# Kernel tuning notes

Measured on AMD Instinct MI355X. Metric: run time of the kernel, lower is better.

Reference implementation:

```python
import jax, jax.numpy as jnp
import numpy as np

DECAY = 0.99
LR = 0.01

def setup_inputs() -> dict:
    key = jax.random.key(0)
    ks = jax.random.split(key, 6)
    B, S, D, M = 4, 4096, 1024, 128
    sD = 1.0 / np.sqrt(D)
    sM = 1.0 / np.sqrt(M)
    return {
        "x": jax.random.normal(ks[0], (B, S, D), dtype=jnp.float32),
        "Wk": jax.random.uniform(ks[1], (M, D), jnp.float32, -sD, sD),
        "bk": jnp.zeros((M,), jnp.float32),
        "Wv": jax.random.uniform(ks[2], (M, D), jnp.float32, -sD, sD),
        "bv": jnp.zeros((M,), jnp.float32),
        "Wq": jax.random.uniform(ks[3], (M, D), jnp.float32, -sD, sD),
        "bq": jnp.zeros((M,), jnp.float32),
        "Wo": jax.random.uniform(ks[4], (D, M), jnp.float32, -sM, sM),
        "bo": jnp.zeros((D,), jnp.float32),
    }

def reference(x, Wk, bk, Wv, bv, Wq, bq, Wo, bo):
    B, S, D = x.shape
    M = Wk.shape[0]
    # Precompute all projections in one batched GEMM each: [B,S,M]
    k = jnp.einsum('bsd,md->bsm', x, Wk) + bk
    v = jnp.einsum('bsd,md->bsm', x, Wv) + bv
    q = jnp.einsum('bsd,md->bsm', x, Wq) + bq

    def step(state, kvq):
        k_t, v_t, q_t = kvq  # each [B, M]
        # readout uses the PRE-update state, matching the torch loop order
        out_t = jnp.einsum('bij,bj->bi', state, q_t)          # [B, M]
        state = DECAY * state + LR * jnp.einsum('bi,bj->bij', v_t, k_t)
        return state, out_t

    state0 = jnp.zeros((B, M, M), x.dtype)
    # scan over time: move seq axis to front -> [S, B, M]
    xs = (jnp.swapaxes(k, 0, 1), jnp.swapaxes(v, 0, 1), jnp.swapaxes(q, 0, 1))
    state, outs = jax.lax.scan(step, state0, xs)
    outs = jnp.swapaxes(outs, 0, 1)                            # [B, S, M]
    y = jnp.einsum('bsm,dm->bsd', outs, Wo) + bo               # [B, S, D]
    return (y, state)
```

## Files before the change

### kernel.cpp

```cpp
#include <hip/hip_runtime.h>
#include <math.h>

namespace {
constexpr int kB = 4;
constexpr int kS = 4096;
constexpr int kD = 1024;
constexpr int kM = 128;
constexpr int kC = 64;
constexpr int kNC = kS / kC;
constexpr int kRS = kB * kS;
constexpr float kLR = 0.01f;
constexpr float kLog2d = -0.0144995696f;
}

typedef __bf16 bf16x8 __attribute__((ext_vector_type(8)));
typedef float  f32x4  __attribute__((ext_vector_type(4)));
typedef unsigned short u16;
typedef unsigned int   u32;

__device__ __forceinline__ u16 f2bf(float f) {
  u32 x = __float_as_uint(f);
  u32 r = (x + 0x7fffu + ((x >> 16) & 1u)) >> 16;
  return (u16)r;
}

__device__ __forceinline__ float bf2f(u16 h) {
  return __uint_as_float(((u32)h) << 16);
}

__device__ __forceinline__ void gl_lds16(const void* g, void* l) {
  __builtin_amdgcn_global_load_lds(
      (const __attribute__((address_space(1))) void*)g,
      (__attribute__((address_space(3))) void*)l, 16, 0, 0);
}

__device__ __forceinline__ f32x4 mf(bf16x8 a, bf16x8 b, f32x4 c) {
  return __builtin_amdgcn_mfma_f32_16x16x32_bf16(a, b, c, 0, 0, 0);
}

__global__ __launch_bounds__(256)
void cast_w_kernel(const float* __restrict__ Wk, const float* __restrict__ Wv,
                   const float* __restrict__ Wq, const float* __restrict__ Wo,
                   u16* __restrict__ Wkvq, u16* __restrict__ Woh)
{
  int i = (blockIdx.x * 256 + threadIdx.x) * 4;
  const float* src;
  u16* dst;
  if (i < 393216) {
    src = (i < 131072) ? Wk + i : (i < 262144) ? Wv + (i - 131072) : Wq + (i - 262144);
    dst = Wkvq + i;
  } else {
    src = Wo + (i - 393216);
    dst = Woh + (i - 393216);
  }
  float4 v = *(const float4*)src;
  ushort4 o;
  o.x = f2bf(v.x); o.y = f2bf(v.y); o.z = f2bf(v.z); o.w = f2bf(v.w);
  *(ushort4*)dst = o;
}

__global__ __launch_bounds__(256)
void fused_proj_intra(const float* __restrict__ x, const u16* __restrict__ Wkvq,
                      const float* __restrict__ bk, const float* __restrict__ bv,
                      const float* __restrict__ bq,
                      u16* __restrict__ Qg, u16* __restrict__ O1g,
                      float* __restrict__ SU)
{
  __shared__ __align__(16) u16 L[32768];
  const int c = blockIdx.x, b = blockIdx.y;
  const int R0 = b * kS + c * kC;
  const int tid = threadIdx.x, w = tid >> 6, lane = tid & 63;
  const int fr = lane & 15, qd = lane >> 4;

  f32x4 acc[4][6] = {};
  const int xrow = tid >> 2, xcol = (tid & 3) * 8;
  const float* xp = x + (size_t)(R0 + xrow) * kD + xcol;
  u16* asDst = &L[xrow * 32 + xcol];
  const u16* wp = Wkvq + (size_t)(96 * w + (lane >> 2)) * kD + (lane & 3) * 8;
  u16* bsDst = &L[2048 + (96 * w) * 32];

  float4 xa = *(const float4*)xp;
  float4 xb = *(const float4*)(xp + 4);
  for (int k0 = 0; k0 < kD; k0 += 32) {
    __syncthreads();
#pragma unroll
    for (int i = 0; i < 6; ++i)
      gl_lds16(wp + k0 + (size_t)(i * 16) * kD, bsDst + i * 512);
    u16 xh8[8];
    xh8[0] = f2bf(xa.x); xh8[1] = f2bf(xa.y); xh8[2] = f2bf(xa.z); xh8[3] = f2bf(xa.w);
    xh8[4] = f2bf(xb.x); xh8[5] = f2bf(xb.y); xh8[6] = f2bf(xb.z); xh8[7] = f2bf(xb.w);
    *(uint4*)asDst = *(uint4*)xh8;
    __syncthreads();
    if (k0 + 32 < kD) {
      xa = *(const float4*)(xp + k0 + 32);
      xb = *(const float4*)(xp + k0 + 36);
    }
    bf16x8 av[4], bvv[6];
#pragma unroll
    for (int mi = 0; mi < 4; ++mi)
      av[mi] = *(const bf16x8*)&L[(mi * 16 + fr) * 32 + qd * 8];
#pragma unroll
    for (int nj = 0; nj < 6; ++nj)
      bvv[nj] = *(const bf16x8*)&L[2048 + (96 * w + nj * 16 + fr) * 32 + qd * 8];
#pragma unroll
    for (int mi = 0; mi < 4; ++mi)
#pragma unroll
      for (int nj = 0; nj < 6; ++nj)
        acc[mi][nj] = mf(av[mi], bvv[nj], acc[mi][nj]);
  }
  __syncthreads();

  float dp63[16];
#pragma unroll
  for (int mi = 0; mi < 4; ++mi)
#pragma unroll
    for (int r = 0; r < 4; ++r)
      dp63[mi * 4 + r] = kLR * exp2f((float)(63 - (mi * 16 + qd * 4 + r)) * kLog2d);

#pragma unroll
  for (int nj = 0; nj < 6; ++nj) {
    const int n = 96 * w + nj * 16 + fr;
    const int slab = n >> 7, j = n & 127;
    const float* bp = (slab == 0) ? bk : (slab == 1) ? bv : bq;
    const float bias = bp[j];
#pragma unroll
    for (int mi = 0; mi < 4; ++mi)
#pragma unroll
      for (int r = 0; r < 4; ++r) {
        const int t = mi * 16 + qd * 4 + r;
        const float val = acc[mi][nj][r] + bias;
        const u16 h = f2bf(val);
        if (slab == 0) {
          L[8192 + (j >> 5) * 2048 + t * 32 + (j & 31)] = h;
          L[24576 + (t >> 5) * 4096 + j * 32 + (t & 31)] = f2bf(val * dp63[mi * 4 + r]);
        } else if (slab == 1) {
          L[16384 + (t >> 5) * 4096 + j * 32 + (t & 31)] = h;
        } else {
          L[(j >> 5) * 2048 + t * 32 + (j & 31)] = h;
          Qg[(size_t)(R0 + t) * kM + j] = h;
        }
      }
  }
  __syncthreads();

  const int mP = (w >> 1) * 32, nP = (w & 1) * 32;
  f32x4 p[2][2] = {};
#pragma unroll
  for (int kp = 0; kp < 4; ++kp) {
    bf16x8 a2[2], b2[2];
#pragma unroll
    for (int mi = 0; mi < 2; ++mi)
      a2[mi] = *(const bf16x8*)&L[kp * 2048 + (mP + mi * 16 + fr) * 32 + qd * 8];
#pragma unroll
    for (int ni = 0; ni < 2; ++ni)
      b2[ni] = *(const bf16x8*)&L[8192 + kp * 2048 + (nP + ni * 16 + fr) * 32 + qd * 8];
#pragma unroll
    for (int mi = 0; mi < 2; ++mi)
#pragma unroll
      for (int ni = 0; ni < 2; ++ni)
        p[mi][ni] = mf(a2[mi], b2[ni], p[mi][ni]);
  }
  __syncthreads();

#pragma unroll
  for (int mi = 0; mi < 2; ++mi)
#pragma unroll
    for (int r = 0; r < 4; ++r) {
      const int t = mP + mi * 16 + qd * 4 + r;
#pragma unroll
      for (int ni = 0; ni < 2; ++ni) {
        const int u = nP + ni * 16 + fr;
        float av2 = 0.f;
        if (u < t) av2 = kLR * exp2f((float)(t - 1 - u) * kLog2d) * p[mi][ni][r];
        L[8192 + (u >> 5) * 2048 + t * 32 + (u & 31)] = f2bf(av2);
      }
    }
  __syncthreads();

  const int mO = (w >> 1) * 32, nO = (w & 1) * 64;
  const int mU = (w >> 1) * 64, nU = (w & 1) * 64;
  f32x4 o1[2][4] = {}, uu[4][4] = {};
#pragma unroll
  for (int kp = 0; kp < 2; ++kp) {
    bf16x8 af[2], vb[4], va[4], ub[4];
#pragma unroll
    for (int mi = 0; mi < 2; ++mi)
      af[mi] = *(const bf16x8*)&L[8192 + kp * 2048 + (mO + mi * 16 + fr) * 32 + qd * 8];
#pragma unroll
    for (int ni = 0; ni < 4; ++ni)
      vb[ni] = *(const bf16x8*)&L[16384 + kp * 4096 + (nO + ni * 16 + fr) * 32 + qd * 8];
#pragma unroll
    for (int mi = 0; mi < 4; ++mi)
      va[mi] = *(const bf16x8*)&L[16384 + kp * 4096 + (mU + mi * 16 + fr) * 32 + qd * 8];
#pragma unroll
    for (int ni = 0; ni < 4; ++ni)
      ub[ni] = *(const bf16x8*)&L[24576 + kp * 4096 + (nU + ni * 16 + fr) * 32 + qd * 8];
#pragma unroll
    for (int mi = 0; mi < 2; ++mi)
#pragma unroll
      for (int ni = 0; ni < 4; ++ni)
        o1[mi][ni] = mf(af[mi], vb[ni], o1[mi][ni]);
#pragma unroll
    for (int mi = 0; mi < 4; ++mi)
#pragma unroll
      for (int ni = 0; ni < 4; ++ni)
        uu[mi][ni] = mf(va[mi], ub[ni], uu[mi][ni]);
  }

#pragma unroll
  for (int mi = 0; mi < 2; ++mi)
#pragma unroll
    for (int ni = 0; ni < 4; ++ni)
#pragma unroll
      for (int r = 0; r < 4; ++r) {
        const int t = mO + mi * 16 + qd * 4 + r, i = nO + ni * 16 + fr;
        O1g[(size_t)(R0 + t) * kM + i] = f2bf(o1[mi][ni][r]);
      }
  float* SUc = SU + (size_t)(b * kNC + c) * (kM * kM);
#pragma unroll
  for (int mi = 0; mi < 4; ++mi)
#pragma unroll
    for (int ni = 0; ni < 4; ++ni)
#pragma unroll
      for (int r = 0; r < 4; ++r) {
        const int i = mU + mi * 16 + qd * 4 + r, j = nU + ni * 16 + fr;
        SUc[i * kM + j] = uu[mi][ni][r];
      }
}

__global__ __launch_bounds__(256)
void scan_kernel(const float* __restrict__ SU, u16* __restrict__ Sb16,
                 float* __restrict__ state_out)
{
  const int e = blockIdx.x * 256 + threadIdx.x;
  const int b = e >> 14, ij = e & 16383;
  const float* base = SU + (size_t)b * kNC * 16384 + ij;
  u16* sb = Sb16 + (size_t)b * kNC * 16384 + ij;
  const float dC = exp2f((float)kC * kLog2d);
  float prev = 0.f;
#pragma unroll 8
  for (int c2 = 0; c2 < kNC; ++c2) {
    const float u = base[(size_t)c2 * 16384];
    sb[(size_t)c2 * 16384] = f2bf(prev);
    prev = fmaf(dC, prev, u);
  }
  state_out[e] = prev;
}

__global__ __launch_bounds__(256)
void fused_combine_out(const u16* __restrict__ Qg, const u16* __restrict__ Sb16,
                       const u16* __restrict__ O1g, const u16* __restrict__ Woh,
                       const float* __restrict__ bo, float* __restrict__ y)
{
  __shared__ __align__(16) u16 L[24576];
  const int c = blockIdx.x, b = blockIdx.y;
  const int R0 = b * kS + c * kC;
  const int tid = threadIdx.x, w = tid >> 6, lane = tid & 63;
  const int fr = lane & 15, qd = lane >> 4;
  const size_t cbS = (size_t)(b * kNC + c) * 16384;

  {
    const u16* gq = Qg + (size_t)(R0 + (lane >> 2)) * kM + w * 32 + (lane & 3) * 8;
    u16* lq = &L[w * 2048];
#pragma unroll
    for (int g = 0; g < 4; ++g)
      gl_lds16(gq + (size_t)(g * 16) * kM, lq + g * 512);
    const u16* gs = Sb16 + cbS + (size_t)(lane >> 2) * kM + w * 32 + (lane & 3) * 8;
    u16* ls = &L[8192 + w * 4096];
#pragma unroll
    for (int g = 0; g < 8; ++g)
      gl_lds16(gs + (size_t)(g * 16) * kM, ls + g * 512);
  }

  const int mO = (w >> 1) * 32, nO = (w & 1) * 64;
  u16 o1h[2][4][4];
#pragma unroll
  for (int mi = 0; mi < 2; ++mi)
#pragma unroll
    for (int ni = 0; ni < 4; ++ni)
#pragma unroll
      for (int r = 0; r < 4; ++r)
        o1h[mi][ni][r] =
            O1g[(size_t)(R0 + mO + mi * 16 + qd * 4 + r) * kM + nO + ni * 16 + fr];
  __syncthreads();

  f32x4 o2[2][4] = {};
#pragma unroll
  for (int kp = 0; kp < 4; ++kp) {
    bf16x8 aq[2], bs[4];
#pragma unroll
    for (int mi = 0; mi < 2; ++mi)
      aq[mi] = *(const bf16x8*)&L[kp * 2048 + (mO + mi * 16 + fr) * 32 + qd * 8];
#pragma unroll
    for (int ni = 0; ni < 4; ++ni)
      bs[ni] = *(const bf16x8*)&L[8192 + kp * 4096 + (nO + ni * 16 + fr) * 32 + qd * 8];
#pragma unroll
    for (int mi = 0; mi < 2; ++mi)
#pragma unroll
      for (int ni = 0; ni < 4; ++ni)
        o2[mi][ni] = mf(aq[mi], bs[ni], o2[mi][ni]);
  }
  __syncthreads();

#pragma unroll
  for (int mi = 0; mi < 2; ++mi)
#pragma unroll
    for (int r = 0; r < 4; ++r) {
      const int t = mO + mi * 16 + qd * 4 + r;
      const float dt = exp2f((float)t * kLog2d);
#pragma unroll
      for (int ni = 0; ni < 4; ++ni) {
        const int i = nO + ni * 16 + fr;
        const float ov = fmaf(dt, o2[mi][ni][r], bf2f(o1h[mi][ni][r]));
        L[(i >> 5) * 2048 + t * 32 + (i & 31)] = f2bf(ov);
      }
    }
  __syncthreads();

#pragma unroll 1
  for (int h = 0; h < 2; ++h) {
    const int n0 = w * 256 + h * 128;
    f32x4 fy[4][8] = {};
#pragma unroll
    for (int kp = 0; kp < 4; ++kp) {
      bf16x8 ao[4], bw[8];
#pragma unroll
      for (int mi = 0; mi < 4; ++mi)
        ao[mi] = *(const bf16x8*)&L[kp * 2048 + (mi * 16 + fr) * 32 + qd * 8];
#pragma unroll
      for (int nj = 0; nj < 8; ++nj)
        bw[nj] = *(const bf16x8*)&Woh[(size_t)(n0 + nj * 16 + fr) * kM + kp * 32 + qd * 8];
#pragma unroll
      for (int mi = 0; mi < 4; ++mi)
#pragma unroll
        for (int nj = 0; nj < 8; ++nj)
          fy[mi][nj] = mf(ao[mi], bw[nj], fy[mi][nj]);
    }
#pragma unroll
    for (int nj = 0; nj < 8; ++nj) {
      const int d = n0 + nj * 16 + fr;
      const float bb = bo[d];
#pragma unroll
      for (int mi = 0; mi < 4; ++mi)
#pragma unroll
        for (int r = 0; r < 4; ++r)
          y[(size_t)(R0 + mi * 16 + qd * 4 + r) * kD + d] = fy[mi][nj][r] + bb;
    }
  }
}

extern "C" void kernel_launch(void* const* d_in, const int* in_sizes, int n_in,
                              void* d_out, int out_size, void* d_ws, size_t ws_size,
                              hipStream_t stream) {
  const float* x  = (const float*)d_in[0];
  const float* Wk = (const float*)d_in[1];
  const float* bk = (const float*)d_in[2];
  const float* Wv = (const float*)d_in[3];
  const float* bv = (const float*)d_in[4];
  const float* Wq = (const float*)d_in[5];
  const float* bq = (const float*)d_in[6];
  const float* Wo = (const float*)d_in[7];
  const float* bo = (const float*)d_in[8];

  char* wsp = (char*)d_ws;
  u16* Wkvq = (u16*)wsp;   wsp += (size_t)384 * 1024 * 2;
  u16* Woh  = (u16*)wsp;   wsp += (size_t)1024 * 128 * 2;
  u16* Qg   = (u16*)wsp;   wsp += (size_t)kRS * kM * 2;
  u16* O1g  = (u16*)wsp;   wsp += (size_t)kRS * kM * 2;
  float* SU = (float*)wsp; wsp += (size_t)kB * kNC * 16384 * 4;
  u16* Sb16 = (u16*)wsp;   wsp += (size_t)kB * kNC * 16384 * 2;

  float* y = (float*)d_out;
  float* state_out = y + (size_t)kRS * kD;

  dim3 blk(256);
  cast_w_kernel<<<dim3(512), blk, 0, stream>>>(Wk, Wv, Wq, Wo, Wkvq, Woh);
  fused_proj_intra<<<dim3(kNC, kB), blk, 0, stream>>>(x, Wkvq, bk, bv, bq, Qg, O1g, SU);
  scan_kernel<<<dim3(kB * 16384 / 256), blk, 0, stream>>>(SU, Sb16, state_out);
  fused_combine_out<<<dim3(kNC, kB), blk, 0, stream>>>(Qg, Sb16, O1g, Woh, bo, y);
}
```

Baseline: 189.6 us.

## Split fused projection and combine kernels into finer-grained kernels with fragment layouts

Splits the fused projection+intra-chunk kernel into a projection GEMM with a 256x3 grid that is double-buffered in LDS, plus a separate intra-chunk kernel. It also splits combine+output into a combine kernel and an out-projection GEMM on an 8x128 grid. Intermediates are stored in an MFMA-fragment-ordered layout so the consumer kernels can load them straight into LDS. The aim is more blocks per launch and better pipelining than the 256-block fused kernels. The cost is extra launches and more global round trips for Q, K, V and the intermediate outputs.

```diff
diff --git a/kernel.cpp b/kernel.cpp
--- a/kernel.cpp
+++ b/kernel.cpp
@@ -8,6 +8,7 @@
 constexpr int kM = 128;
 constexpr int kC = 64;
 constexpr int kNC = kS / kC;
+constexpr int kNCG = kB * kNC;
 constexpr int kRS = kB * kS;
 constexpr float kLR = 0.01f;
 constexpr float kLog2d = -0.0144995696f;
@@ -36,6 +37,22 @@
 
 __device__ __forceinline__ f32x4 mf(bf16x8 a, bf16x8 b, f32x4 c) {
   return __builtin_amdgcn_mfma_f32_16x16x32_bf16(a, b, c, 0, 0, 0);
+}
+
+__device__ __forceinline__ ushort4 pack4(float4 a) {
+  ushort4 o;
+  o.x = f2bf(a.x); o.y = f2bf(a.y); o.z = f2bf(a.z); o.w = f2bf(a.w);
+  return o;
+}
+
+__device__ __forceinline__ int fo64x128(int r, int c) {
+  return ((r >> 4) * 4 + (c >> 5)) * 1024 + ((c >> 3) & 3) * 256 + (r & 15) * 16 + (c & 7) * 2;
+}
+__device__ __forceinline__ int fo128x64(int r, int c) {
+  return ((r >> 4) * 2 + (c >> 5)) * 1024 + ((c >> 3) & 3) * 256 + (r & 15) * 16 + (c & 7) * 2;
+}
+__device__ __forceinline__ int fo64x64(int r, int c) {
+  return ((r >> 4) * 2 + (c >> 5)) * 1024 + ((c >> 3) & 3) * 256 + (r & 15) * 16 + (c & 7) * 2;
 }
 
 __global__ __launch_bounds__(256)
@@ -54,177 +71,221 @@
     dst = Woh + (i - 393216);
   }
   float4 v = *(const float4*)src;
-  ushort4 o;
-  o.x = f2bf(v.x); o.y = f2bf(v.y); o.z = f2bf(v.z); o.w = f2bf(v.w);
-  *(ushort4*)dst = o;
-}
-
-__global__ __launch_bounds__(256)
-void fused_proj_intra(const float* __restrict__ x, const u16* __restrict__ Wkvq,
-                      const float* __restrict__ bk, const float* __restrict__ bv,
-                      const float* __restrict__ bq,
-                      u16* __restrict__ Qg, u16* __restrict__ O1g,
-                      float* __restrict__ SU)
-{
-  __shared__ __align__(16) u16 L[32768];
-  const int c = blockIdx.x, b = blockIdx.y;
-  const int R0 = b * kS + c * kC;
+  *(ushort4*)dst = pack4(v);
+}
+
+__global__ __launch_bounds__(256, 3)
+void proj_gemm(const float* __restrict__ x, const u16* __restrict__ Wkvq,
+               const float* __restrict__ bk, const float* __restrict__ bv,
+               const float* __restrict__ bq,
+               u16* __restrict__ Qg, u16* __restrict__ Kg,
+               u16* __restrict__ VTg, u16* __restrict__ KwTg)
+{
+  __shared__ __align__(16) u16 L[24576];
+  const int cg = blockIdx.x, s = blockIdx.y;
+  const int R0 = cg * 64;
   const int tid = threadIdx.x, w = tid >> 6, lane = tid & 63;
   const int fr = lane & 15, qd = lane >> 4;
-
-  f32x4 acc[4][6] = {};
-  const int xrow = tid >> 2, xcol = (tid & 3) * 8;
-  const float* xp = x + (size_t)(R0 + xrow) * kD + xcol;
-  u16* asDst = &L[xrow * 32 + xcol];
-  const u16* wp = Wkvq + (size_t)(96 * w + (lane >> 2)) * kD + (lane & 3) * 8;
-  u16* bsDst = &L[2048 + (96 * w) * 32];
-
-  float4 xa = *(const float4*)xp;
-  float4 xb = *(const float4*)(xp + 4);
-  for (int k0 = 0; k0 < kD; k0 += 32) {
+  const int wr = w >> 1, wc = w & 1;
+
+  constexpr int A0 = 0, A1o = 8192, B0 = 16384, B1o = 32768;
+
+  const int xr = tid >> 2, s4 = tid & 3;
+  const float* xp = x + (size_t)(R0 + xr) * kD + s4 * 4;
+  int aoffq[4];
+#pragma unroll
+  for (int q = 0; q < 4; ++q)
+    aoffq[q] = ((xr >> 4) * 2 + (q >> 1)) * 1024 + (((s4 >> 1) + 2 * q) & 3) * 256
+             + (xr & 15) * 16 + (s4 & 1) * 8;
+
+  const u16* wbase = Wkvq + (size_t)(128 * s) * kD + qd * 8;
+
+  f32x4 acc[2][4] = {};
+  float4 xv[4];
+
+  {
+#pragma unroll
+    for (int g = 0; g < 4; ++g) {
+      const int pn = 4 * w + g, ng = pn >> 1, kh = pn & 1;
+      gl_lds16(wbase + (size_t)(ng * 16 + fr) * kD + kh * 32, &L[(B0 + pn * 1024) >> 1]);
+    }
+    float4 x0[4];
+#pragma unroll
+    for (int q = 0; q < 4; ++q) x0[q] = *(const float4*)(xp + q * 16);
+#pragma unroll
+    for (int q = 0; q < 4; ++q) *(ushort4*)&L[(A0 + aoffq[q]) >> 1] = pack4(x0[q]);
+#pragma unroll
+    for (int q = 0; q < 4; ++q) xv[q] = *(const float4*)(xp + 64 + q * 16);
+  }
+  __syncthreads();
+
+#pragma unroll 2
+  for (int i = 0; i < 16; ++i) {
+    const int Ac = (i & 1) ? A1o : A0, Bc = (i & 1) ? B1o : B0;
+    const int An = (i & 1) ? A0 : A1o, Bn = (i & 1) ? B0 : B1o;
+    if (i < 15) {
+      const int k1 = (i + 1) * 64;
+#pragma unroll
+      for (int g = 0; g < 4; ++g) {
+        const int pn = 4 * w + g, ng = pn >> 1, kh = pn & 1;
+        gl_lds16(wbase + (size_t)(ng * 16 + fr) * kD + k1 + kh * 32, &L[(Bn + pn * 1024) >> 1]);
+      }
+#pragma unroll
+      for (int q = 0; q < 4; ++q) *(ushort4*)&L[(An + aoffq[q]) >> 1] = pack4(xv[q]);
+      if (i < 14) {
+#pragma unroll
+        for (int q = 0; q < 4; ++q) xv[q] = *(const float4*)(xp + (i + 2) * 64 + q * 16);
+      }
+    }
+    bf16x8 af[2][2], bfr[2][4];
+#pragma unroll
+    for (int kh = 0; kh < 2; ++kh) {
+#pragma unroll
+      for (int mi = 0; mi < 2; ++mi)
+        af[kh][mi] = *(const bf16x8*)&L[(Ac + ((wr * 2 + mi) * 2 + kh) * 1024 + qd * 256 + fr * 16) >> 1];
+#pragma unroll
+      for (int ng = 0; ng < 4; ++ng)
+        bfr[kh][ng] = *(const bf16x8*)&L[(Bc + ((wc * 4 + ng) * 2 + kh) * 1024 + qd * 256 + fr * 16) >> 1];
+    }
+#pragma unroll
+    for (int kh = 0; kh < 2; ++kh)
+#pragma unroll
+      for (int mi = 0; mi < 2; ++mi)
+#pragma unroll
+        for (int ng = 0; ng < 4; ++ng)
+          acc[mi][ng] = mf(af[kh][mi], bfr[kh][ng], acc[mi][ng]);
     __syncthreads();
-#pragma unroll
-    for (int i = 0; i < 6; ++i)
-      gl_lds16(wp + k0 + (size_t)(i * 16) * kD, bsDst + i * 512);
-    u16 xh8[8];
-    xh8[0] = f2bf(xa.x); xh8[1] = f2bf(xa.y); xh8[2] = f2bf(xa.z); xh8[3] = f2bf(xa.w);
-    xh8[4] = f2bf(xb.x); xh8[5] = f2bf(xb.y); xh8[6] = f2bf(xb.z); xh8[7] = f2bf(xb.w);
-    *(uint4*)asDst = *(uint4*)xh8;
-    __syncthreads();
-    if (k0 + 32 < kD) {
-      xa = *(const float4*)(xp + k0 + 32);
-      xb = *(const float4*)(xp + k0 + 36);
-    }
-    bf16x8 av[4], bvv[6];
-#pragma unroll
-    for (int mi = 0; mi < 4; ++mi)
-      av[mi] = *(const bf16x8*)&L[(mi * 16 + fr) * 32 + qd * 8];
-#pragma unroll
-    for (int nj = 0; nj < 6; ++nj)
-      bvv[nj] = *(const bf16x8*)&L[2048 + (96 * w + nj * 16 + fr) * 32 + qd * 8];
-#pragma unroll
-    for (int mi = 0; mi < 4; ++mi)
-#pragma unroll
-      for (int nj = 0; nj < 6; ++nj)
-        acc[mi][nj] = mf(av[mi], bvv[nj], acc[mi][nj]);
-  }
-  __syncthreads();
-
-  float dp63[16];
-#pragma unroll
-  for (int mi = 0; mi < 4; ++mi)
-#pragma unroll
-    for (int r = 0; r < 4; ++r)
-      dp63[mi * 4 + r] = kLR * exp2f((float)(63 - (mi * 16 + qd * 4 + r)) * kLog2d);
-
-#pragma unroll
-  for (int nj = 0; nj < 6; ++nj) {
-    const int n = 96 * w + nj * 16 + fr;
-    const int slab = n >> 7, j = n & 127;
-    const float* bp = (slab == 0) ? bk : (slab == 1) ? bv : bq;
-    const float bias = bp[j];
-#pragma unroll
-    for (int mi = 0; mi < 4; ++mi)
+  }
+
+  const float* bp = (s == 0) ? bk : (s == 1) ? bv : bq;
+  float bias[4];
+#pragma unroll
+  for (int ng = 0; ng < 4; ++ng) bias[ng] = bp[wc * 64 + ng * 16 + fr];
+  const size_t cb = (size_t)cg * 8192;
+
+  if (s == 0) {
+    float dp[2][4];
+#pragma unroll
+    for (int mi = 0; mi < 2; ++mi)
+#pragma unroll
+      for (int r = 0; r < 4; ++r)
+        dp[mi][r] = kLR * exp2f((float)(63 - (wr * 32 + mi * 16 + qd * 4 + r)) * kLog2d);
+#pragma unroll
+    for (int mi = 0; mi < 2; ++mi)
+#pragma unroll
+      for (int ng = 0; ng < 4; ++ng)
+#pragma unroll
+        for (int r = 0; r < 4; ++r) {
+          const int t = wr * 32 + mi * 16 + qd * 4 + r, n = wc * 64 + ng * 16 + fr;
+          const float v = acc[mi][ng][r] + bias[ng];
+          Kg[cb + (fo64x128(t, n) >> 1)] = f2bf(v);
+          KwTg[cb + (fo128x64(n, t) >> 1)] = f2bf(v * dp[mi][r]);
+        }
+  } else if (s == 1) {
+#pragma unroll
+    for (int mi = 0; mi < 2; ++mi)
+#pragma unroll
+      for (int ng = 0; ng < 4; ++ng)
+#pragma unroll
+        for (int r = 0; r < 4; ++r) {
+          const int t = wr * 32 + mi * 16 + qd * 4 + r, n = wc * 64 + ng * 16 + fr;
+          VTg[cb + (fo128x64(n, t) >> 1)] = f2bf(acc[mi][ng][r] + bias[ng]);
+        }
+  } else {
+#pragma unroll
+    for (int mi = 0; mi < 2; ++mi)
+#pragma unroll
+      for (int ng = 0; ng < 4; ++ng)
+#pragma unroll
+        for (int r = 0; r < 4; ++r) {
+          const int t = wr * 32 + mi * 16 + qd * 4 + r, n = wc * 64 + ng * 16 + fr;
+          Qg[cb + (fo64x128(t, n) >> 1)] = f2bf(acc[mi][ng][r] + bias[ng]);
+        }
+  }
+}
+
+__global__ __launch_bounds__(256, 2)
+void intra_kernel(const u16* __restrict__ Qg, const u16* __restrict__ Kg,
+                  const u16* __restrict__ VTg, const u16* __restrict__ KwTg,
+                  u16* __restrict__ O1g, float* __restrict__ SU)
+{
+  __shared__ __align__(16) u16 L[32768];
+  const int cg = blockIdx.x;
+  const int tid = threadIdx.x, w = tid >> 6, lane = tid & 63;
+  const int fr = lane & 15, qd = lane >> 4;
+  const size_t cb = (size_t)cg * 8192;
+
+#pragma unroll
+  for (int g = 0; g < 4; ++g) {
+    const int pn = 4 * w + g;
+    gl_lds16(Qg + cb + pn * 512 + lane * 8, &L[(0 + pn * 1024) >> 1]);
+    gl_lds16(Kg + cb + pn * 512 + lane * 8, &L[(16384 + pn * 1024) >> 1]);
+    gl_lds16(VTg + cb + pn * 512 + lane * 8, &L[(32768 + pn * 1024) >> 1]);
+    gl_lds16(KwTg + cb + pn * 512 + lane * 8, &L[(49152 + pn * 1024) >> 1]);
+  }
+  __syncthreads();
+
+  f32x4 p[4] = {};
+#pragma unroll
+  for (int kc = 0; kc < 4; ++kc) {
+    bf16x8 aq = *(const bf16x8*)&L[(0 + (w * 4 + kc) * 1024 + qd * 256 + fr * 16) >> 1];
+#pragma unroll
+    for (int ug = 0; ug < 4; ++ug) {
+      bf16x8 bkf = *(const bf16x8*)&L[(16384 + (ug * 4 + kc) * 1024 + qd * 256 + fr * 16) >> 1];
+      p[ug] = mf(aq, bkf, p[ug]);
+    }
+  }
+  __syncthreads();
+
+#pragma unroll
+  for (int ug = 0; ug < 4; ++ug)
+#pragma unroll
+    for (int r = 0; r < 4; ++r) {
+      const int t = w * 16 + qd * 4 + r, u = ug * 16 + fr;
+      float av = 0.f;
+      if (u < t) av = kLR * exp2f((float)(t - 1 - u) * kLog2d) * p[ug][r];
+      L[(0 + fo64x64(t, u)) >> 1] = f2bf(av);
+    }
+  __syncthreads();
+
+  f32x4 o1[8] = {}, uu[2][8] = {};
+#pragma unroll
+  for (int h = 0; h < 2; ++h) {
+    bf16x8 aA = *(const bf16x8*)&L[(0 + (w * 2 + h) * 1024 + qd * 256 + fr * 16) >> 1];
+    bf16x8 aV[2];
+#pragma unroll
+    for (int mi = 0; mi < 2; ++mi)
+      aV[mi] = *(const bf16x8*)&L[(32768 + ((2 * w + mi) * 2 + h) * 1024 + qd * 256 + fr * 16) >> 1];
+#pragma unroll
+    for (int ig = 0; ig < 8; ++ig) {
+      bf16x8 bV = *(const bf16x8*)&L[(32768 + (ig * 2 + h) * 1024 + qd * 256 + fr * 16) >> 1];
+      o1[ig] = mf(aA, bV, o1[ig]);
+    }
+#pragma unroll
+    for (int jg = 0; jg < 8; ++jg) {
+      bf16x8 bK = *(const bf16x8*)&L[(49152 + (jg * 2 + h) * 1024 + qd * 256 + fr * 16) >> 1];
+#pragma unroll
+      for (int mi = 0; mi < 2; ++mi)
+        uu[mi][jg] = mf(aV[mi], bK, uu[mi][jg]);
+    }
+  }
+
+#pragma unroll
+  for (int ig = 0; ig < 8; ++ig)
+#pragma unroll
+    for (int r = 0; r < 4; ++r) {
+      const int t = w * 16 + qd * 4 + r, i2 = ig * 16 + fr;
+      O1g[cb + (fo64x128(t, i2) >> 1)] = f2bf(o1[ig][r]);
+    }
+  float* SUc = SU + (size_t)cg * 16384;
+#pragma unroll
+  for (int mi = 0; mi < 2; ++mi)
+#pragma unroll
+    for (int jg = 0; jg < 8; ++jg)
 #pragma unroll
       for (int r = 0; r < 4; ++r) {
-        const int t = mi * 16 + qd * 4 + r;
-        const float val = acc[mi][nj][r] + bias;
-        const u16 h = f2bf(val);
-        if (slab == 0) {
-          L[8192 + (j >> 5) * 2048 + t * 32 + (j & 31)] = h;
-          L[24576 + (t >> 5) * 4096 + j * 32 + (t & 31)] = f2bf(val * dp63[mi * 4 + r]);
-        } else if (slab == 1) {
-          L[16384 + (t >> 5) * 4096 + j * 32 + (t & 31)] = h;
-        } else {
-          L[(j >> 5) * 2048 + t * 32 + (j & 31)] = h;
-          Qg[(size_t)(R0 + t) * kM + j] = h;
-        }
-      }
-  }
-  __syncthreads();
-
-  const int mP = (w >> 1) * 32, nP = (w & 1) * 32;
-  f32x4 p[2][2] = {};
-#pragma unroll
-  for (int kp = 0; kp < 4; ++kp) {
-    bf16x8 a2[2], b2[2];
-#pragma unroll
-    for (int mi = 0; mi < 2; ++mi)
-      a2[mi] = *(const bf16x8*)&L[kp * 2048 + (mP + mi * 16 + fr) * 32 + qd * 8];
-#pragma unroll
-    for (int ni = 0; ni < 2; ++ni)
-      b2[ni] = *(const bf16x8*)&L[8192 + kp * 2048 + (nP + ni * 16 + fr) * 32 + qd * 8];
-#pragma unroll
-    for (int mi = 0; mi < 2; ++mi)
-#pragma unroll
-      for (int ni = 0; ni < 2; ++ni)
-        p[mi][ni] = mf(a2[mi], b2[ni], p[mi][ni]);
-  }
-  __syncthreads();
-
-#pragma unroll
-  for (int mi = 0; mi < 2; ++mi)
-#pragma unroll
-    for (int r = 0; r < 4; ++r) {
-      const int t = mP + mi * 16 + qd * 4 + r;
-#pragma unroll
-      for (int ni = 0; ni < 2; ++ni) {
-        const int u = nP + ni * 16 + fr;
-        float av2 = 0.f;
-        if (u < t) av2 = kLR * exp2f((float)(t - 1 - u) * kLog2d) * p[mi][ni][r];
-        L[8192 + (u >> 5) * 2048 + t * 32 + (u & 31)] = f2bf(av2);
-      }
-    }
-  __syncthreads();
-
-  const int mO = (w >> 1) * 32, nO = (w & 1) * 64;
-  const int mU = (w >> 1) * 64, nU = (w & 1) * 64;
-  f32x4 o1[2][4] = {}, uu[4][4] = {};
-#pragma unroll
-  for (int kp = 0; kp < 2; ++kp) {
-    bf16x8 af[2], vb[4], va[4], ub[4];
-#pragma unroll
-    for (int mi = 0; mi < 2; ++mi)
-      af[mi] = *(const bf16x8*)&L[8192 + kp * 2048 + (mO + mi * 16 + fr) * 32 + qd * 8];
-#pragma unroll
-    for (int ni = 0; ni < 4; ++ni)
-      vb[ni] = *(const bf16x8*)&L[16384 + kp * 4096 + (nO + ni * 16 + fr) * 32 + qd * 8];
-#pragma unroll
-    for (int mi = 0; mi < 4; ++mi)
-      va[mi] = *(const bf16x8*)&L[16384 + kp * 4096 + (mU + mi * 16 + fr) * 32 + qd * 8];
-#pragma unroll
-    for (int ni = 0; ni < 4; ++ni)
-      ub[ni] = *(const bf16x8*)&L[24576 + kp * 4096 + (nU + ni * 16 + fr) * 32 + qd * 8];
-#pragma unroll
-    for (int mi = 0; mi < 2; ++mi)
-#pragma unroll
-      for (int ni = 0; ni < 4; ++ni)
-        o1[mi][ni] = mf(af[mi], vb[ni], o1[mi][ni]);
-#pragma unroll
-    for (int mi = 0; mi < 4; ++mi)
-#pragma unroll
-      for (int ni = 0; ni < 4; ++ni)
-        uu[mi][ni] = mf(va[mi], ub[ni], uu[mi][ni]);
-  }
-
-#pragma unroll
-  for (int mi = 0; mi < 2; ++mi)
-#pragma unroll
-    for (int ni = 0; ni < 4; ++ni)
-#pragma unroll
-      for (int r = 0; r < 4; ++r) {
-        const int t = mO + mi * 16 + qd * 4 + r, i = nO + ni * 16 + fr;
-        O1g[(size_t)(R0 + t) * kM + i] = f2bf(o1[mi][ni][r]);
-      }
-  float* SUc = SU + (size_t)(b * kNC + c) * (kM * kM);
-#pragma unroll
-  for (int mi = 0; mi < 4; ++mi)
-#pragma unroll
-    for (int ni = 0; ni < 4; ++ni)
-#pragma unroll
-      for (int r = 0; r < 4; ++r) {
-        const int i = mU + mi * 16 + qd * 4 + r, j = nU + ni * 16 + fr;
-        SUc[i * kM + j] = uu[mi][ni][r];
+        const int i2 = w * 32 + mi * 16 + qd * 4 + r, j = jg * 16 + fr;
+        SUc[i2 * kM + j] = uu[mi][jg][r];
       }
 }
 
@@ -247,105 +308,102 @@
   state_out[e] = prev;
 }
 
-__global__ __launch_bounds__(256)
-void fused_combine_out(const u16* __restrict__ Qg, const u16* __restrict__ Sb16,
-                       const u16* __restrict__ O1g, const u16* __restrict__ Woh,
-                       const float* __restrict__ bo, float* __restrict__ y)
-{
-  __shared__ __align__(16) u16 L[24576];
-  const int c = blockIdx.x, b = blockIdx.y;
-  const int R0 = b * kS + c * kC;
+__global__ __launch_bounds__(256, 2)
+void combine_kernel(const u16* __restrict__ Qg, const u16* __restrict__ Sb16,
+                    const u16* __restrict__ O1g, u16* __restrict__ Outg)
+{
+  __shared__ __align__(16) u16 L[32768];
+  const int cg = blockIdx.x;
   const int tid = threadIdx.x, w = tid >> 6, lane = tid & 63;
   const int fr = lane & 15, qd = lane >> 4;
-  const size_t cbS = (size_t)(b * kNC + c) * 16384;
-
-  {
-    const u16* gq = Qg + (size_t)(R0 + (lane >> 2)) * kM + w * 32 + (lane & 3) * 8;
-    u16* lq = &L[w * 2048];
-#pragma unroll
-    for (int g = 0; g < 4; ++g)
-      gl_lds16(gq + (size_t)(g * 16) * kM, lq + g * 512);
-    const u16* gs = Sb16 + cbS + (size_t)(lane >> 2) * kM + w * 32 + (lane & 3) * 8;
-    u16* ls = &L[8192 + w * 4096];
-#pragma unroll
-    for (int g = 0; g < 8; ++g)
-      gl_lds16(gs + (size_t)(g * 16) * kM, ls + g * 512);
-  }
-
-  const int mO = (w >> 1) * 32, nO = (w & 1) * 64;
-  u16 o1h[2][4][4];
-#pragma unroll
-  for (int mi = 0; mi < 2; ++mi)
-#pragma unroll
-    for (int ni = 0; ni < 4; ++ni)
-#pragma unroll
-      for (int r = 0; r < 4; ++r)
-        o1h[mi][ni][r] =
-            O1g[(size_t)(R0 + mO + mi * 16 + qd * 4 + r) * kM + nO + ni * 16 + fr];
-  __syncthreads();
-
-  f32x4 o2[2][4] = {};
-#pragma unroll
-  for (int kp = 0; kp < 4; ++kp) {
-    bf16x8 aq[2], bs[4];
-#pragma unroll
-    for (int mi = 0; mi < 2; ++mi)
-      aq[mi] = *(const bf16x8*)&L[kp * 2048 + (mO + mi * 16 + fr) * 32 + qd * 8];
-#pragma unroll
-    for (int ni = 0; ni < 4; ++ni)
-      bs[ni] = *(const bf16x8*)&L[8192 + kp * 4096 + (nO + ni * 16 + fr) * 32 + qd * 8];
-#pragma unroll
-    for (int mi = 0; mi < 2; ++mi)
-#pragma unroll
-      for (int ni = 0; ni < 4; ++ni)
-        o2[mi][ni] = mf(aq[mi], bs[ni], o2[mi][ni]);
-  }
-  __syncthreads();
-
-#pragma unroll
-  for (int mi = 0; mi < 2; ++mi)
+  const size_t cb = (size_t)cg * 8192;
+  const u16* Sbc = Sb16 + (size_t)cg * 16384;
+
+#pragma unroll
+  for (int g = 0; g < 4; ++g) {
+    const int pn = 4 * w + g;
+    gl_lds16(Qg + cb + pn * 512 + lane * 8, &L[(0 + pn * 1024) >> 1]);
+    gl_lds16(O1g + cb + pn * 512 + lane * 8, &L[(49152 + pn * 1024) >> 1]);
+  }
+#pragma unroll
+  for (int g = 0; g < 8; ++g) {
+    const int pn = 8 * w + g, ig = pn >> 2, kc = pn & 3;
+    gl_lds16(Sbc + (size_t)(ig * 16 + fr) * kM + kc * 32 + qd * 8,
+             &L[(16384 + pn * 1024) >> 1]);
+  }
+  __syncthreads();
+
+  f32x4 o2[8] = {};
+#pragma unroll
+  for (int kc = 0; kc < 4; ++kc) {
+    bf16x8 aq = *(const bf16x8*)&L[(0 + (w * 4 + kc) * 1024 + qd * 256 + fr * 16) >> 1];
+#pragma unroll
+    for (int ig = 0; ig < 8; ++ig) {
+      bf16x8 bS = *(const bf16x8*)&L[(16384 + (ig * 4 + kc) * 1024 + qd * 256 + fr * 16) >> 1];
+      o2[ig] = mf(aq, bS, o2[ig]);
+    }
+  }
+
+  float dt[4];
+#pragma unroll
+  for (int r = 0; r < 4; ++r) dt[r] = exp2f((float)(w * 16 + qd * 4 + r) * kLog2d);
+#pragma unroll
+  for (int ig = 0; ig < 8; ++ig)
 #pragma unroll
     for (int r = 0; r < 4; ++r) {
-      const int t = mO + mi * 16 + qd * 4 + r;
-      const float dt = exp2f((float)t * kLog2d);
-#pragma unroll
-      for (int ni = 0; ni < 4; ++ni) {
-        const int i = nO + ni * 16 + fr;
-        const float ov = fmaf(dt, o2[mi][ni][r], bf2f(o1h[mi][ni][r]));
-        L[(i >> 5) * 2048 + t * 32 + (i & 31)] = f2bf(ov);
+      const int t = w * 16 + qd * 4 + r, i2 = ig * 16 + fr;
+      const float o1v = bf2f(L[(49152 + fo64x128(t, i2)) >> 1]);
+      Outg[cb + (fo64x128(t, i2) >> 1)] = f2bf(fmaf(dt[r], o2[ig][r], o1v));
+    }
+}
+
+__global__ __launch_bounds__(256, 2)
+void out_gemm(const u16* __restrict__ Outg, const u16* __restrict__ Woh,
+              const float* __restrict__ bo, float* __restrict__ y)
+{
+  __shared__ __align__(16) u16 L[32768];
+  const int dg = blockIdx.x, rg = blockIdx.y;
+  const int tid = threadIdx.x, w = tid >> 6, lane = tid & 63;
+  const int fr = lane & 15, qd = lane >> 4;
+  const size_t ab = (size_t)rg * 16384;
+
+#pragma unroll
+  for (int g = 0; g < 8; ++g) {
+    const int pn = 8 * w + g;
+    gl_lds16(Outg + ab + pn * 512 + lane * 8, &L[(0 + pn * 1024) >> 1]);
+    const int pg = pn >> 2, kc = pn & 3;
+    gl_lds16(Woh + (size_t)(dg * 128 + pg * 16 + fr) * kM + kc * 32 + qd * 8,
+             &L[(32768 + pn * 1024) >> 1]);
+  }
+  __syncthreads();
+
+  f32x4 acc[2][8] = {};
+#pragma unroll
+  for (int kc = 0; kc < 4; ++kc) {
+    bf16x8 aA[2];
+#pragma unroll
+    for (int mi = 0; mi < 2; ++mi)
+      aA[mi] = *(const bf16x8*)&L[(((w * 2 + mi) * 4 + kc) * 1024 + qd * 256 + fr * 16) >> 1];
+#pragma unroll
+    for (int nj = 0; nj < 8; ++nj) {
+      bf16x8 bB = *(const bf16x8*)&L[(32768 + (nj * 4 + kc) * 1024 + qd * 256 + fr * 16) >> 1];
+#pragma unroll
+      for (int mi = 0; mi < 2; ++mi)
+        acc[mi][nj] = mf(aA[mi], bB, acc[mi][nj]);
+    }
+  }
+
+#pragma unroll
+  for (int nj = 0; nj < 8; ++nj) {
+    const int d = dg * 128 + nj * 16 + fr;
+    const float bb = bo[d];
+#pragma unroll
+    for (int mi = 0; mi < 2; ++mi)
+#pragma unroll
+      for (int r = 0; r < 4; ++r) {
+        const int row = rg * 128 + w * 32 + mi * 16 + qd * 4 + r;
+        y[(size_t)row * kD + d] = acc[mi][nj][r] + bb;
       }
-    }
-  __syncthreads();
-
-#pragma unroll 1
-  for (int h = 0; h < 2; ++h) {
-    const int n0 = w * 256 + h * 128;
-    f32x4 fy[4][8] = {};
-#pragma unroll
-    for (int kp = 0; kp < 4; ++kp) {
-      bf16x8 ao[4], bw[8];
-#pragma unroll
-      for (int mi = 0; mi < 4; ++mi)
-        ao[mi] = *(const bf16x8*)&L[kp * 2048 + (mi * 16 + fr) * 32 + qd * 8];
-#pragma unroll
-      for (int nj = 0; nj < 8; ++nj)
-        bw[nj] = *(const bf16x8*)&Woh[(size_t)(n0 + nj * 16 + fr) * kM + kp * 32 + qd * 8];
-#pragma unroll
-      for (int mi = 0; mi < 4; ++mi)
-#pragma unroll
-        for (int nj = 0; nj < 8; ++nj)
-          fy[mi][nj] = mf(ao[mi], bw[nj], fy[mi][nj]);
-    }
-#pragma unroll
-    for (int nj = 0; nj < 8; ++nj) {
-      const int d = n0 + nj * 16 + fr;
-      const float bb = bo[d];
-#pragma unroll
-      for (int mi = 0; mi < 4; ++mi)
-#pragma unroll
-        for (int r = 0; r < 4; ++r)
-          y[(size_t)(R0 + mi * 16 + qd * 4 + r) * kD + d] = fy[mi][nj][r] + bb;
-    }
   }
 }
 
@@ -363,19 +421,25 @@
   const float* bo = (const float*)d_in[8];
 
   char* wsp = (char*)d_ws;
-  u16* Wkvq = (u16*)wsp;   wsp += (size_t)384 * 1024 * 2;
-  u16* Woh  = (u16*)wsp;   wsp += (size_t)1024 * 128 * 2;
-  u16* Qg   = (u16*)wsp;   wsp += (size_t)kRS * kM * 2;
-  u16* O1g  = (u16*)wsp;   wsp += (size_t)kRS * kM * 2;
-  float* SU = (float*)wsp; wsp += (size_t)kB * kNC * 16384 * 4;
-  u16* Sb16 = (u16*)wsp;   wsp += (size_t)kB * kNC * 16384 * 2;
+  u16* Wkvq = (u16*)wsp;  wsp += (size_t)384 * 1024 * 2;
+  u16* Woh  = (u16*)wsp;  wsp += (size_t)1024 * 128 * 2;
+  u16* Qg   = (u16*)wsp;  wsp += (size_t)kNCG * 8192 * 2;
+  u16* Kg   = (u16*)wsp;  wsp += (size_t)kNCG * 8192 * 2;
+  u16* Outg = Kg;
+  u16* VTg  = (u16*)wsp;
+  u16* KwTg = VTg + (size_t)kNCG * 8192;
+  u16* Sb16 = VTg;
+  wsp += (size_t)kNCG * 16384 * 2;
+  u16* O1g  = (u16*)wsp;  wsp += (size_t)kNCG * 8192 * 2;
+  float* SU = (float*)wsp; wsp += (size_t)kNCG * 16384 * 4;
 
   float* y = (float*)d_out;
   float* state_out = y + (size_t)kRS * kD;
 
-  dim3 blk(256);
-  cast_w_kernel<<<dim3(512), blk, 0, stream>>>(Wk, Wv, Wq, Wo, Wkvq, Woh);
-  fused_proj_intra<<<dim3(kNC, kB), blk, 0, stream>>>(x, Wkvq, bk, bv, bq, Qg, O1g, SU);
-  scan_kernel<<<dim3(kB * 16384 / 256), blk, 0, stream>>>(SU, Sb16, state_out);
-  fused_combine_out<<<dim3(kNC, kB), blk, 0, stream>>>(Qg, Sb16, O1g, Woh, bo, y);
-}
+  cast_w_kernel<<<dim3(512), dim3(256), 0, stream>>>(Wk, Wv, Wq, Wo, Wkvq, Woh);
+  proj_gemm<<<dim3(kNCG, 3), dim3(256), 0, stream>>>(x, Wkvq, bk, bv, bq, Qg, Kg, VTg, KwTg);
+  intra_kernel<<<dim3(kNCG), dim3(256), 0, stream>>>(Qg, Kg, VTg, KwTg, O1g, SU);
+  scan_kernel<<<dim3(kB * 16384 / 256), dim3(256), 0, stream>>>(SU, Sb16, state_out);
+  combine_kernel<<<dim3(kNCG), dim3(256), 0, stream>>>(Qg, Sb16, O1g, Outg);
+  out_gemm<<<dim3(8, 128), dim3(256), 0, stream>>>(Outg, Woh, bo, y);
+}
```

After: 188.5 us. Within noise of the previous version (-0.6%).
